# Kernel tuning notes

Hardware: AMD Instinct MI355X
Metric: run time of the kernel (lower is better)

The kernel has to match this reference:

```python
import jax, jax.numpy as jnp
import numpy as np
import math

B, D, N, H, NHEADS, NCLS = 4096, 256, 256, 1, 4, 10


def conv(x, w, b, stride, pad):
    y = jax.lax.conv_general_dilated(x, w, (stride, stride), [(pad, pad), (pad, pad)],
                                     dimension_numbers=('NCHW', 'OIHW', 'NCHW'))
    return y + b[None, :, None, None]


def cdist(z, c):
    # z: [B, D], c: [N, D] -> Euclidean distance [B, N]
    d2 = jnp.sum(z * z, -1)[:, None] + jnp.sum(c * c, -1)[None, :] - 2.0 * (z @ c.T)
    return jnp.sqrt(jnp.maximum(d2, 0.0))


def setup_inputs() -> dict:
    key = jax.random.key(0)
    ks = jax.random.split(key, 32)
    s = 0.02
    inp = {
        'x': jax.random.normal(ks[0], (B, 3, 32, 32), jnp.float32),
        'y': jax.random.randint(ks[1], (B,), 0, NCLS),
        'conv1_w': jax.random.normal(ks[2], (32, 3, 5, 5), jnp.float32) * s,
        'conv1_b': jnp.zeros((32,), jnp.float32),
        'conv2_w': jax.random.normal(ks[3], (64, 32, 3, 3), jnp.float32) * s,
        'conv2_b': jnp.zeros((64,), jnp.float32),
        'conv3_w': jax.random.normal(ks[4], (128, 64, 3, 3), jnp.float32) * s,
        'conv3_b': jnp.zeros((128,), jnp.float32),
        'conv4_w': jax.random.normal(ks[5], (256, 128, 3, 3), jnp.float32) * s,
        'conv4_b': jnp.zeros((256,), jnp.float32),
        'enc_w': jax.random.normal(ks[6], (256 * 8 * 8, D), jnp.float32) * s,
        'enc_b': jnp.zeros((D,), jnp.float32),
        'class_emb': jax.random.normal(ks[7], (NCLS, D), jnp.float32),
        'node_emb': jax.random.normal(ks[8], (N_NODES := 1, D), jnp.float32),
        'query_w': jax.random.normal(ks[9], (D, D), jnp.float32) * s,
        'query_b': jnp.zeros((D,), jnp.float32),
        'attn_w': jax.random.normal(ks[10], (D, D * NHEADS), jnp.float32) * s,
        'attn_b': jnp.zeros((D * NHEADS,), jnp.float32),
        'clf_w': jax.random.normal(ks[11], (D * NHEADS, NCLS), jnp.float32) * s,
        'clf_b': jnp.zeros((NCLS,), jnp.float32),
        'node_fc_w': jax.random.normal(ks[12], (D, D), jnp.float32) * s,
        'node_fc_b': jnp.zeros((D,), jnp.float32),
        'protos': jax.random.normal(ks[13], (N, D), jnp.float32),
        'grid_pos': jax.random.normal(ks[14], (N, D), jnp.float32),
        'temp_raw': jnp.array([math.log(0.95 / 0.05)], jnp.float32),
        'gate_logits': jnp.zeros((N,), jnp.float32),
    }
    return inp


def reference(x, y, conv1_w, conv1_b, conv2_w, conv2_b, conv3_w, conv3_b,
              conv4_w, conv4_b, enc_w, enc_b, class_emb, node_emb,
              query_w, query_b, attn_w, attn_b, clf_w, clf_b,
              node_fc_w, node_fc_b, protos, grid_pos, temp_raw, gate_logits):
    # shared encoder: conv stack -> flatten -> linear, 32x32 -> 8x8
    h1 = jax.nn.relu(conv(x, conv1_w, conv1_b, 2, 1))    # [B,32,15,15]
    h2 = jax.nn.relu(conv(h1, conv2_w, conv2_b, 2, 1))   # [B,64,8,8]
    h3 = jax.nn.relu(conv(h2, conv3_w, conv3_b, 1, 1))   # [B,128,8,8]
    h4 = jax.nn.relu(conv(h3, conv4_w, conv4_b, 1, 1))   # [B,256,8,8]
    z0 = h4.reshape(x.shape[0], -1) @ enc_w + enc_b      # [B,D]

    # Node: encoder_fc + SoftSOM (cdist + cdist -> softmax -> gate -> renorm -> blend)
    z = z0 @ node_fc_w + node_fc_b
    temp = jax.nn.sigmoid(temp_raw[0]) * (1.0 - 0.001) + 0.001
    d_total = cdist(z, protos) + cdist(z, grid_pos)      # [B,N]
    w = jax.nn.softmax(-d_total / temp, axis=-1) * jax.nn.sigmoid(gate_logits)[None, :]
    w = w / (w.sum(-1, keepdims=True) + 1e-8)
    blended = w @ protos                                 # [B,D]

    # node attention over n_nodes=1
    topo_stack = blended[:, None, :]                     # [B,1,D]
    query = class_emb[y] @ query_w + query_b             # [B,D]
    proj = (node_emb @ attn_w + attn_b).reshape(node_emb.shape[0], NHEADS, D)  # [n,h,D]
    attn_logits = jnp.einsum('bd,nhd->bhn', query, proj)
    attn_w_ = jax.nn.softmax(attn_logits, axis=-1)
    fused = jnp.einsum('bhn,bnd->bhd', attn_w_, topo_stack).reshape(x.shape[0], NHEADS * D)
    logits = fused @ clf_w + clf_b                       # [B,10]
    return logits
```

## Files before the change

kernel.cpp:

```cpp
#include <hip/hip_runtime.h>
#include <math.h>

#define TPB 256

typedef __attribute__((ext_vector_type(8))) short bf16x8;
typedef __attribute__((ext_vector_type(4))) float f32x4;
typedef __attribute__((ext_vector_type(2))) float f32x2;

#define OFF_PN2   0
#define OFF_GN2   256
#define OFF_GATE  512
#define OFF_TEMP  768
#define OFF_WEFF  1024
#define OFF_W1T   3584
#define OFF_W2T_BYTES 737280ul
#define OFF_W3T_BYTES 786432ul
#define OFF_W4T_BYTES 983040ul
#define OFF_EWT_BYTES 2097152ul
#define OFF_NFWT_BYTES 10485760ul
#define OFF_PJD_BYTES  10616832ul
#define OFF_GJD_BYTES  10747904ul
#define OFF_PTB_BYTES  10878976ul
#define OFF_A_BYTES   12582912ul
#define OFF_B_BYTES   (OFF_A_BYTES + 67108864ul)
#define OFF_Z0_BYTES  (OFF_B_BYTES + 33554432ul)

__device__ __forceinline__ float bf2f(ushort u) {
  return __uint_as_float(((unsigned)u) << 16);
}
__device__ __forceinline__ ushort f2bf(float f) {
  unsigned x = __float_as_uint(f);
  return (ushort)((x + 0x7fffu + ((x >> 16) & 1u)) >> 16);
}
__device__ __forceinline__ unsigned pack2(float a, float b) {
  return (unsigned)f2bf(a) | ((unsigned)f2bf(b) << 16);
}

__device__ __forceinline__ void gload_lds16(const ushort* g, ushort* l) {
  __builtin_amdgcn_global_load_lds(
      (const __attribute__((address_space(1))) unsigned int*)g,
      (__attribute__((address_space(3))) unsigned int*)l, 16, 0, 0);
}

__device__ __forceinline__ float block_sum(float v, float* red) {
  #pragma unroll
  for (int off = 32; off > 0; off >>= 1) v += __shfl_down(v, off, 64);
  int wid = threadIdx.x >> 6;
  __syncthreads();
  if ((threadIdx.x & 63) == 0) red[wid] = v;
  __syncthreads();
  return red[0] + red[1] + red[2] + red[3];
}

__global__ void __launch_bounds__(256) k_init(
    const float* __restrict__ ew,    ushort* __restrict__ ewt,
    const float* __restrict__ w1,    const float* __restrict__ w2,
    const float* __restrict__ w3,    const float* __restrict__ w4,
    float* __restrict__ w1t, ushort* __restrict__ w2t,
    ushort* __restrict__ w3t, ushort* __restrict__ w4t,
    const float* __restrict__ protos, const float* __restrict__ gridp,
    const float* __restrict__ gate_logits, const float* __restrict__ temp_raw,
    const float* __restrict__ clf_w, float* __restrict__ ws,
    const float* __restrict__ nfw, ushort* __restrict__ nfwt,
    ushort* __restrict__ pjd, ushort* __restrict__ gjd,
    ushort* __restrict__ ptb) {
  __shared__ float tile[64][65];
  __shared__ float red[4];
  const int bx = blockIdx.x, t = threadIdx.x;

  if (bx < 1024) {
    int kb = bx & 255, nb = bx >> 8;
    #pragma unroll
    for (int i = 0; i < 16; ++i) {
      int idx = t + i*256, k = idx >> 6, n = idx & 63;
      tile[k][n] = ew[(size_t)(kb*64 + k)*256 + nb*64 + n];
    }
    __syncthreads();
    #pragma unroll
    for (int i = 0; i < 16; ++i) {
      int idx = t + i*256, n = idx >> 6, k = idx & 63;
      ewt[(size_t)(nb*64 + n)*16384 + kb*64 + k] = f2bf(tile[k][n]);
    }
    return;
  }
  if (bx < 2176) {
    int idx = (bx - 1024)*256 + t;
    if (idx < 2400) {
      int tap = idx >> 5, oc = idx & 31;
      w1t[idx] = w1[oc*75 + tap];
    }
    if (idx < 18432) {
      int tap = idx >> 11, r = idx & 2047, oc = r >> 5, ic = r & 31;
      w2t[idx] = f2bf(w2[oc*288 + ic*9 + tap]);
    }
    if (idx < 73728) {
      int tap = idx >> 13, r = idx & 8191, oc = r >> 6, ic = r & 63;
      w3t[idx] = f2bf(w3[oc*576 + ic*9 + tap]);
    }
    if (idx < 294912) {
      int tap = idx >> 15, r = idx & 32767, oc = r >> 7, ic = r & 127;
      w4t[idx] = f2bf(w4[oc*1152 + ic*9 + tap]);
    }
    return;
  }
  if (bx < 2432) {
    int b = bx - 2176;
    float pv = protos[b*256 + t];
    float gv = gridp [b*256 + t];
    float sp = block_sum(pv*pv, red);
    float sg = block_sum(gv*gv, red);
    if (t == 0) {
      ws[OFF_PN2 + b] = sp;
      ws[OFF_GN2 + b] = sg;
      ws[OFF_GATE + b] = 1.f/(1.f + expf(-gate_logits[b]));
    }
    if (b == 0) {
      for (int i = t; i < 2560; i += TPB) {
        int d = i/10, c = i%10;
        ws[OFF_WEFF + i] = clf_w[d*10+c] + clf_w[(256+d)*10+c]
                         + clf_w[(512+d)*10+c] + clf_w[(768+d)*10+c];
      }
      if (t == 0) {
        float s = 1.f/(1.f + expf(-temp_raw[0]));
        ws[OFF_TEMP] = s*(1.f - 0.001f) + 0.001f;
      }
    }
    return;
  }
  {
    int idx = (bx - 2432)*256 + t;
    int a = idx >> 8, b = idx & 255;
    nfwt[idx] = f2bf(nfw[b*256 + a]);
    pjd [idx] = f2bf(protos[idx]);
    gjd [idx] = f2bf(gridp[idx]);
    ptb [idx] = f2bf(protos[b*256 + a]);
  }
}

__global__ void __launch_bounds__(256) k_conv12(const float* __restrict__ x,
    const float* __restrict__ w1t, const float* __restrict__ b1,
    const ushort* __restrict__ w2t, const float* __restrict__ b2,
    ushort* __restrict__ h2c) {
  __shared__ ushort xs[17*17*40];
  __shared__ float  xf[3*32*33];
  int b = blockIdx.x, t = threadIdx.x;
  for (int i = t; i < 5780; i += TPB) ((unsigned*)xs)[i] = 0u;
  const float* xb = x + (size_t)b*3072;
  #pragma unroll
  for (int i = 0; i < 3; ++i) {
    int idx = (t + i*256)*4;
    float4 v = *(const float4*)&xb[idx];
    int ic = idx >> 10, rem = idx & 1023, iy = rem >> 5, ix = rem & 31;
    float* dst = &xf[ic*1056 + iy*33 + ix];
    dst[0] = v.x; dst[1] = v.y; dst[2] = v.z; dst[3] = v.w;
  }
  __syncthreads();

  if (t < 225) {
    int oy = t/15, ox = t%15;
    f32x2 acc[16];
    #pragma unroll
    for (int o = 0; o < 16; ++o) acc[o] = *(const f32x2*)&b1[2*o];
    for (int ic = 0; ic < 3; ++ic) {
      const int icb = ic*1056;
      #pragma unroll
      for (int ky = 0; ky < 5; ++ky) {
        int iy = 2*oy - 1 + ky;
        bool rok = (unsigned)iy < 32u;
        int rbase = icb + (rok ? iy*33 : 0);
        #pragma unroll
        for (int kx = 0; kx < 5; ++kx) {
          int ix = 2*ox - 1 + kx;
          bool ok = rok && ((unsigned)ix < 32u);
          float xv = xf[rbase + (ok ? ix : 0)];
          xv = ok ? xv : 0.f;
          f32x2 xv2 = {xv, xv};
          const float* wrow = &w1t[(ic*25 + ky*5 + kx)*32];
          #pragma unroll
          for (int g = 0; g < 8; ++g) {
            f32x2 wlo = {wrow[4*g+0], wrow[4*g+1]};
            f32x2 whi = {wrow[4*g+2], wrow[4*g+3]};
            acc[2*g]   += xv2*wlo;
            acc[2*g+1] += xv2*whi;
          }
        }
      }
    }
    unsigned pk[16];
    #pragma unroll
    for (int g = 0; g < 16; ++g)
      pk[g] = pack2(fmaxf(acc[g].x, 0.f), fmaxf(acc[g].y, 0.f));
    ushort* cell = &xs[((oy+1)*17 + (ox+1))*40];
    #pragma unroll
    for (int q = 0; q < 4; ++q) *(uint4*)(cell + q*8) = ((uint4*)pk)[q];
  }
  __syncthreads();

  const int lane = t & 63, w = t >> 6;
  const int quad = lane >> 4, row16 = lane & 15;
  f32x4 acc2[4];
  #pragma unroll
  for (int mt = 0; mt < 4; ++mt) acc2[mt] = (f32x4)0.f;
  #pragma unroll
  for (int ky = 0; ky < 3; ++ky)
    #pragma unroll
    for (int kx = 0; kx < 3; ++kx) {
      int tap = ky*3 + kx;
      bf16x8 bf = *(const bf16x8*)&w2t[tap*2048 + (w*16 + row16)*32 + quad*8];
      #pragma unroll
      for (int mt = 0; mt < 4; ++mt) {
        int px = mt*16 + row16;
        int iy = 2*(px >> 3) + ky, ix = 2*(px & 7) + kx;
        bf16x8 af = *(const bf16x8*)&xs[(iy*17 + ix)*40 + quad*8];
        acc2[mt] = __builtin_amdgcn_mfma_f32_16x16x32_bf16(bf, af, acc2[mt], 0, 0, 0);
      }
    }
  float4 bb = *(const float4*)&b2[w*16 + quad*4];
  #pragma unroll
  for (int mt = 0; mt < 4; ++mt) {
    int px = mt*16 + row16;
    uint2 dd;
    dd.x = pack2(fmaxf(acc2[mt][0] + bb.x, 0.f), fmaxf(acc2[mt][1] + bb.y, 0.f));
    dd.y = pack2(fmaxf(acc2[mt][2] + bb.z, 0.f), fmaxf(acc2[mt][3] + bb.w, 0.f));
    *(uint2*)&h2c[(size_t)b*4096 + px*64 + w*16 + quad*4] = dd;
  }
}

__global__ void __launch_bounds__(256, 2) k_conv34(const ushort* __restrict__ h2c,
    const float* __restrict__ b3, const float* __restrict__ b4,
    const ushort* __restrict__ w3t, const ushort* __restrict__ w4t,
    ushort* __restrict__ h4c, int img_base) {
  __shared__ __attribute__((aligned(16))) ushort buf[27200];
  ushort* xp  = buf;
  ushort* h3p = buf;
  const int bl = blockIdx.x, t = threadIdx.x;

  for (int i = t; i < 648; i += 256) {
    int img = (i >= 324), r = i - img*324;
    int row = r/9, c = r - row*9;
    int rr = (row < 20) ? ((row < 10) ? row : row + 80)
                        : (((row-20) >> 1) + 1)*10 + ((row-20) & 1)*9;
    *(uint4*)&xp[img*7200 + rr*72 + c*8] = (uint4){0,0,0,0};
  }
  #pragma unroll
  for (int u = 0; u < 4; ++u) {
    int i = t + u*256;
    int img = i >> 9, px = (i >> 3) & 63, icg = i & 7;
    bf16x8 v = *(const bf16x8*)&h2c[(size_t)(img_base + bl*2 + img)*4096 + px*64 + icg*8];
    int row = ((px >> 3) + 1)*10 + (px & 7) + 1;
    *(bf16x8*)&xp[img*7200 + row*72 + icg*8] = v;
  }
  __syncthreads();

  const int lane = t & 63, w = t >> 6;
  const int quad = lane >> 4, row16 = lane & 15;

  int b3off[8], b4off[8], r11c[8];
  #pragma unroll
  for (int mt = 0; mt < 8; ++mt) {
    int px = (mt & 3)*16 + row16;
    int r00 = (px >> 3)*10 + (px & 7);
    int img = mt >> 2;
    b3off[mt] = img*7200  + r00*72  + quad*8;
    b4off[mt] = img*13600 + r00*136 + quad*8;
    r11c[mt]  = img*13600 + (r00 + 11)*136;
  }

  const int ocb3 = w*32;
  f32x4 c3[8][2];
  #pragma unroll
  for (int mt = 0; mt < 8; ++mt) { c3[mt][0] = (f32x4)0.f; c3[mt][1] = (f32x4)0.f; }
  const ushort* w3b = w3t + (ocb3 + row16)*64 + quad*8;
  bf16x8 wa0 = *(const bf16x8*)(w3b);
  bf16x8 wa1 = *(const bf16x8*)(w3b + 1024);
  #pragma unroll
  for (int tap = 0; tap < 9; ++tap) {
    const int t72 = ((tap/3)*10 + (tap%3))*72;
    #pragma unroll
    for (int ks = 0; ks < 2; ++ks) {
      const ushort* wn = w3b + ((ks == 0) ? (tap*8192 + 32) : ((tap+1)*8192));
      bf16x8 n0 = *(const bf16x8*)(wn);
      bf16x8 n1 = *(const bf16x8*)(wn + 1024);
      #pragma unroll
      for (int mt = 0; mt < 8; ++mt) {
        bf16x8 af = *(const bf16x8*)&xp[b3off[mt] + t72 + ks*32];
        c3[mt][0] = __builtin_amdgcn_mfma_f32_16x16x32_bf16(wa0, af, c3[mt][0], 0, 0, 0);
        c3[mt][1] = __builtin_amdgcn_mfma_f32_16x16x32_bf16(wa1, af, c3[mt][1], 0, 0, 0);
      }
      wa0 = n0; wa1 = n1;
    }
  }
  __syncthreads();

  for (int i = t; i < 1224; i += 256) {
    int img2 = (i >= 612), r = i - img2*612;
    int row = r/17, c = r - row*17;
    int rr = (row < 20) ? ((row < 10) ? row : row + 80)
                        : (((row-20) >> 1) + 1)*10 + ((row-20) & 1)*9;
    *(uint4*)&h3p[img2*13600 + rr*136 + c*8] = (uint4){0,0,0,0};
  }
  #pragma unroll
  for (int nt = 0; nt < 2; ++nt) {
    float4 bb = *(const float4*)&b3[ocb3 + nt*16 + quad*4];
    #pragma unroll
    for (int mt = 0; mt < 8; ++mt) {
      uint2 dd;
      dd.x = pack2(fmaxf(c3[mt][nt][0] + bb.x, 0.f), fmaxf(c3[mt][nt][1] + bb.y, 0.f));
      dd.y = pack2(fmaxf(c3[mt][nt][2] + bb.z, 0.f), fmaxf(c3[mt][nt][3] + bb.w, 0.f));
      *(uint2*)&h3p[r11c[mt] + ocb3 + nt*16 + quad*4] = dd;
    }
  }
  __syncthreads();

  const int ocb4 = w*64;
  f32x4 c4[8][4];
  #pragma unroll
  for (int mt = 0; mt < 8; ++mt)
    #pragma unroll
    for (int nt = 0; nt < 4; ++nt) c4[mt][nt] = (f32x4)0.f;
  const ushort* w4b = w4t + (ocb4 + row16)*128 + quad*8;
  bf16x8 r4[4];
  #pragma unroll
  for (int nt = 0; nt < 4; ++nt) r4[nt] = *(const bf16x8*)(w4b + nt*2048);
  #pragma unroll
  for (int tap = 0; tap < 9; ++tap) {
    const int t136 = ((tap/3)*10 + (tap%3))*136;
    #pragma unroll
    for (int ks = 0; ks < 4; ++ks) {
      const ushort* wn = w4b + ((ks < 3) ? (tap*32768 + (ks+1)*32) : ((tap+1)*32768));
      bf16x8 nx[4];
      #pragma unroll
      for (int nt = 0; nt < 4; ++nt) nx[nt] = *(const bf16x8*)(wn + nt*2048);
      #pragma unroll
      for (int mt = 0; mt < 8; ++mt) {
        bf16x8 ax = *(const bf16x8*)&h3p[b4off[mt] + t136 + ks*32];
        #pragma unroll
        for (int nt = 0; nt < 4; ++nt)
          c4[mt][nt] = __builtin_amdgcn_mfma_f32_16x16x32_bf16(ax, r4[nt], c4[mt][nt], 0, 0, 0);
      }
      #pragma unroll
      for (int nt = 0; nt < 4; ++nt) r4[nt] = nx[nt];
    }
  }
  #pragma unroll
  for (int nt = 0; nt < 4; ++nt) {
    int oc = ocb4 + nt*16 + row16;
    float bv = b4[oc];
    #pragma unroll
    for (int mt = 0; mt < 8; ++mt) {
      int ig = bl*2 + (mt >> 2);
      int px0 = (mt & 3)*16 + quad*4;
      uint2 dd;
      dd.x = pack2(fmaxf(c4[mt][nt][0] + bv, 0.f), fmaxf(c4[mt][nt][1] + bv, 0.f));
      dd.y = pack2(fmaxf(c4[mt][nt][2] + bv, 0.f), fmaxf(c4[mt][nt][3] + bv, 0.f));
      *(uint2*)&h4c[(size_t)ig*16384 + oc*64 + px0] = dd;
    }
  }
}

__global__ void __launch_bounds__(512) k_enc(const ushort* __restrict__ h4c,
    const ushort* __restrict__ ewt, float* __restrict__ z0p) {
  __shared__ ushort a_s[2][128*64];
  __shared__ ushort b_s[2][128*64];
  const int t = threadIdx.x, bid = blockIdx.x;
  const int slice = bid & 7;
  const int mb    = (bid >> 3) & 15;
  const int nb    = bid >> 7;
  const int M0 = mb*128, N0 = nb*128;
  const int kbase = slice*2048;
  const int lane = t & 63, wv = t >> 6;
  const int quad = lane >> 4, row16 = lane & 15;
  const int mrow0 = (wv & 3)*32, ncol0 = (wv >> 2)*64;
  const int sr = lane >> 3, sp = lane & 7;

  f32x4 acc[2][4];
  #pragma unroll
  for (int mt = 0; mt < 2; ++mt)
    #pragma unroll
    for (int nt = 0; nt < 4; ++nt) acc[mt][nt] = (f32x4)0.f;

  #pragma unroll
  for (int u = 0; u < 2; ++u) {
    int r = wv*16 + u*8 + sr;
    int c = sp ^ (r & 7);
    gload_lds16(&h4c[(size_t)(M0 + r)*16384 + kbase + c*8], &a_s[0][(wv*16 + u*8)*64]);
    gload_lds16(&ewt[(size_t)(N0 + r)*16384 + kbase + c*8], &b_s[0][(wv*16 + u*8)*64]);
  }
  __syncthreads();

  int cur = 0;
  for (int kt = 0; kt < 32; ++kt) {
    if (kt < 31) {
      const int k1 = kbase + (kt + 1)*64;
      #pragma unroll
      for (int u = 0; u < 2; ++u) {
        int r = wv*16 + u*8 + sr;
        int c = sp ^ (r & 7);
        gload_lds16(&h4c[(size_t)(M0 + r)*16384 + k1 + c*8], &a_s[cur^1][(wv*16 + u*8)*64]);
        gload_lds16(&ewt[(size_t)(N0 + r)*16384 + k1 + c*8], &b_s[cur^1][(wv*16 + u*8)*64]);
      }
    }
    #pragma unroll
    for (int ks = 0; ks < 2; ++ks) {
      bf16x8 af[2], bf[4];
      #pragma unroll
      for (int mt = 0; mt < 2; ++mt) {
        int r = mrow0 + mt*16 + row16;
        int p = (ks*4 + quad) ^ (r & 7);
        af[mt] = *(const bf16x8*)&a_s[cur][r*64 + p*8];
      }
      #pragma unroll
      for (int nt = 0; nt < 4; ++nt) {
        int r = ncol0 + nt*16 + row16;
        int p = (ks*4 + quad) ^ (r & 7);
        bf[nt] = *(const bf16x8*)&b_s[cur][r*64 + p*8];
      }
      #pragma unroll
      for (int mt = 0; mt < 2; ++mt)
        #pragma unroll
        for (int nt = 0; nt < 4; ++nt)
          acc[mt][nt] = __builtin_amdgcn_mfma_f32_16x16x32_bf16(af[mt], bf[nt], acc[mt][nt], 0, 0, 0);
    }
    __syncthreads();
    cur ^= 1;
  }
  #pragma unroll
  for (int mt = 0; mt < 2; ++mt) {
    int il = M0 + mrow0 + mt*16 + quad*4;
    #pragma unroll
    for (int nt = 0; nt < 4; ++nt) {
      int col = N0 + ncol0 + nt*16 + row16;
      #pragma unroll
      for (int r = 0; r < 4; ++r)
        z0p[((size_t)slice*2048 + il + r)*256 + col] = acc[mt][nt][r];
    }
  }
}

__global__ void __launch_bounds__(256) k_post2(const float* __restrict__ zp,
    const float* __restrict__ enc_b, const float* __restrict__ nfb,
    const ushort* __restrict__ nfwt, const ushort* __restrict__ pjd,
    const ushort* __restrict__ gjd, const ushort* __restrict__ ptb,
    const float* __restrict__ ws, const float* __restrict__ clf_b,
    float* __restrict__ out) {
  __shared__ ushort zin[16*264];
  __shared__ ushort zS [16*264];
  __shared__ float  Df [16*264];
  __shared__ ushort wS [16*264];
  __shared__ float  weffS[2560];
  __shared__ float  gateS[256], pnS[256], gnS[256];
  __shared__ float  z2s[16];
  const int t = threadIdx.x, bx = blockIdx.x;
  const int img0 = bx*16;
  gateS[t] = ws[OFF_GATE + t];
  pnS[t]   = ws[OFF_PN2 + t];
  gnS[t]   = ws[OFF_GN2 + t];
  #pragma unroll
  for (int u = 0; u < 10; ++u)
    weffS[t + u*256] = ws[OFF_WEFF + t + u*256];
  #pragma unroll
  for (int u = 0; u < 16; ++u) {
    int i = t + u*256;
    int im = i >> 8, d = i & 255;
    int img = img0 + im;
    int cc = img >> 11, il = img & 2047;
    const float* zb = zp + (size_t)cc*4194304 + (size_t)il*256 + d;
    float s = enc_b[d];
    #pragma unroll
    for (int s8 = 0; s8 < 8; ++s8) s += zb[(size_t)s8*524288];
    zin[im*264 + d] = f2bf(s);
  }
  __syncthreads();

  const int lane = t & 63, w = t >> 6;
  const int quad = lane >> 4, row16 = lane & 15;
  const int n0 = w*64;

  f32x4 zC[4];
  #pragma unroll
  for (int nt = 0; nt < 4; ++nt) zC[nt] = (f32x4)0.f;
  #pragma unroll
  for (int ks = 0; ks < 8; ++ks) {
    bf16x8 az = *(const bf16x8*)&zin[row16*264 + ks*32 + quad*8];
    #pragma unroll
    for (int nt = 0; nt < 4; ++nt) {
      bf16x8 bw = *(const bf16x8*)&nfwt[(n0 + nt*16 + row16)*256 + ks*32 + quad*8];
      zC[nt] = __builtin_amdgcn_mfma_f32_16x16x32_bf16(az, bw, zC[nt], 0, 0, 0);
    }
  }
  #pragma unroll
  for (int nt = 0; nt < 4; ++nt) {
    int n = n0 + nt*16 + row16;
    float nb = nfb[n];
    #pragma unroll
    for (int r = 0; r < 4; ++r)
      zS[(quad*4 + r)*264 + n] = f2bf(zC[nt][r] + nb);
  }
  __syncthreads();

  {
    int im = t >> 4, jg = t & 15;
    float s = 0.f;
    #pragma unroll
    for (int q = 0; q < 16; ++q) {
      float v = bf2f(zS[im*264 + jg + 16*q]);
      s += v*v;
    }
    #pragma unroll
    for (int off = 8; off; off >>= 1) s += __shfl_xor(s, off, 16);
    if (jg == 0) z2s[im] = s;
  }
  __syncthreads();

  f32x4 dpC[4], dgC[4];
  #pragma unroll
  for (int nt = 0; nt < 4; ++nt) { dpC[nt] = (f32x4)0.f; dgC[nt] = (f32x4)0.f; }
  #pragma unroll
  for (int ks = 0; ks < 8; ++ks) {
    bf16x8 az = *(const bf16x8*)&zS[row16*264 + ks*32 + quad*8];
    #pragma unroll
    for (int nt = 0; nt < 4; ++nt) {
      int j = n0 + nt*16 + row16;
      bf16x8 bp = *(const bf16x8*)&pjd[j*256 + ks*32 + quad*8];
      bf16x8 bg = *(const bf16x8*)&gjd[j*256 + ks*32 + quad*8];
      dpC[nt] = __builtin_amdgcn_mfma_f32_16x16x32_bf16(az, bp, dpC[nt], 0, 0, 0);
      dgC[nt] = __builtin_amdgcn_mfma_f32_16x16x32_bf16(az, bg, dgC[nt], 0, 0, 0);
    }
  }
  {
    float temp = ws[OFF_TEMP];
    #pragma unroll
    for (int nt = 0; nt < 4; ++nt) {
      int j = n0 + nt*16 + row16;
      float pn = pnS[j], gn = gnS[j];
      #pragma unroll
      for (int r = 0; r < 4; ++r) {
        int im = quad*4 + r;
        float z2 = z2s[im];
        float d2p = z2 + pn - 2.f*dpC[nt][r];
        float d2g = z2 + gn - 2.f*dgC[nt][r];
        float l = -(sqrtf(fmaxf(d2p, 0.f)) + sqrtf(fmaxf(d2g, 0.f)))/temp;
        Df[im*264 + j] = l;
      }
    }
  }
  __syncthreads();

  {
    int im = t >> 4, jg = t & 15;
    float m = -1e30f;
    #pragma unroll
    for (int q = 0; q < 16; ++q) m = fmaxf(m, Df[im*264 + jg + 16*q]);
    #pragma unroll
    for (int off = 8; off; off >>= 1) m = fmaxf(m, __shfl_xor(m, off, 16));
    float E = 0.f, S = 0.f, ev[16], gv[16];
    #pragma unroll
    for (int q = 0; q < 16; ++q) {
      int j = jg + 16*q;
      float e = expf(Df[im*264 + j] - m);
      float g = gateS[j];
      ev[q] = e; gv[q] = g;
      E += e; S += e*g;
    }
    #pragma unroll
    for (int off = 8; off; off >>= 1) {
      E += __shfl_xor(E, off, 16);
      S += __shfl_xor(S, off, 16);
    }
    float inv = 1.f/(S + 1e-8f*E);
    #pragma unroll
    for (int q = 0; q < 16; ++q)
      wS[im*264 + jg + 16*q] = f2bf(ev[q]*gv[q]*inv);
  }
  __syncthreads();

  f32x4 blC[4];
  #pragma unroll
  for (int nt = 0; nt < 4; ++nt) blC[nt] = (f32x4)0.f;
  #pragma unroll
  for (int ks = 0; ks < 8; ++ks) {
    bf16x8 aw = *(const bf16x8*)&wS[row16*264 + ks*32 + quad*8];
    #pragma unroll
    for (int nt = 0; nt < 4; ++nt) {
      bf16x8 bp = *(const bf16x8*)&ptb[(n0 + nt*16 + row16)*256 + ks*32 + quad*8];
      blC[nt] = __builtin_amdgcn_mfma_f32_16x16x32_bf16(aw, bp, blC[nt], 0, 0, 0);
    }
  }
  #pragma unroll
  for (int nt = 0; nt < 4; ++nt) {
    int d = n0 + nt*16 + row16;
    #pragma unroll
    for (int r = 0; r < 4; ++r)
      Df[(quad*4 + r)*264 + d] = blC[nt][r];
  }
  __syncthreads();

  if (t < 160) {
    int im = t/10, c = t - im*10;
    float s = clf_b[c];
    for (int d = 0; d < 256; ++d)
      s += Df[im*264 + d]*weffS[d*10 + c];
    out[(size_t)(img0 + im)*10 + c] = s;
  }
}

extern "C" void kernel_launch(void* const* d_in, const int* in_sizes, int n_in,
                              void* d_out, int out_size, void* d_ws, size_t ws_size,
                              hipStream_t stream) {
  (void)in_sizes; (void)n_in; (void)out_size; (void)ws_size;
  const float* x      = (const float*)d_in[0];
  const float* c1w    = (const float*)d_in[2];
  const float* c1b    = (const float*)d_in[3];
  const float* c2w    = (const float*)d_in[4];
  const float* c2b    = (const float*)d_in[5];
  const float* c3w    = (const float*)d_in[6];
  const float* c3b    = (const float*)d_in[7];
  const float* c4w    = (const float*)d_in[8];
  const float* c4b    = (const float*)d_in[9];
  const float* encw   = (const float*)d_in[10];
  const float* encb   = (const float*)d_in[11];
  const float* clfw   = (const float*)d_in[18];
  const float* clfb   = (const float*)d_in[19];
  const float* nfw    = (const float*)d_in[20];
  const float* nfb    = (const float*)d_in[21];
  const float* protos = (const float*)d_in[22];
  const float* gridp  = (const float*)d_in[23];
  const float* traw   = (const float*)d_in[24];
  const float* gatel  = (const float*)d_in[25];

  float*  ws   = (float*)d_ws;
  float*  w1t  = ws + OFF_W1T;
  ushort* w2t  = (ushort*)((char*)d_ws + OFF_W2T_BYTES);
  ushort* w3t  = (ushort*)((char*)d_ws + OFF_W3T_BYTES);
  ushort* w4t  = (ushort*)((char*)d_ws + OFF_W4T_BYTES);
  ushort* ewt  = (ushort*)((char*)d_ws + OFF_EWT_BYTES);
  ushort* nfwt = (ushort*)((char*)d_ws + OFF_NFWT_BYTES);
  ushort* pjd  = (ushort*)((char*)d_ws + OFF_PJD_BYTES);
  ushort* gjd  = (ushort*)((char*)d_ws + OFF_GJD_BYTES);
  ushort* ptb  = (ushort*)((char*)d_ws + OFF_PTB_BYTES);
  ushort* h4c  = (ushort*)((char*)d_ws + OFF_A_BYTES);
  ushort* h2c  = (ushort*)((char*)d_ws + OFF_B_BYTES);
  float*  zp   = (float*) ((char*)d_ws + OFF_B_BYTES);
  float*  out  = (float*)d_out;

  hipLaunchKernelGGL(k_init, dim3(2688), dim3(TPB), 0, stream,
                     encw, ewt, c1w, c2w, c3w, c4w, w1t, w2t, w3t, w4t,
                     protos, gridp, gatel, traw, clfw, ws,
                     nfw, nfwt, pjd, gjd, ptb);
  hipLaunchKernelGGL(k_conv12, dim3(4096), dim3(TPB), 0, stream, x, w1t, c1b, w2t, c2b, h2c);
  for (int c = 0; c < 2; ++c) {
    hipLaunchKernelGGL(k_conv34, dim3(1024), dim3(TPB), 0, stream,
                       h2c, c3b, c4b, w3t, w4t, h4c, c*2048);
    hipLaunchKernelGGL(k_enc, dim3(256), dim3(512), 0, stream,
                       h4c, ewt, zp + (size_t)c*4194304);
  }
  hipLaunchKernelGGL(k_post2, dim3(256), dim3(TPB), 0, stream,
                     zp, encb, nfb, nfwt, pjd, gjd, ptb, ws, clfb, out);
}
```

Measured before the change: 495.2 us.

## Co-schedule second half of conv1-2 with first conv3-4 chunk in one launch

The conv1/conv2 stage is split into two halves of 2048 images. The second half runs inside the same grid as the first conv3/conv4 chunk, with block index selecting which body runs, so the two independent stages can occupy the GPU together instead of running back to back. Conv bodies are moved into inline device functions so both kernels can share them. The trade-off is that conv1/conv2 blocks in the fused kernel reserve the larger conv3/conv4 shared-memory footprint and inherit its launch bounds, which may lower their occupancy.

```diff
diff --git a/kernel.cpp b/kernel.cpp
--- a/kernel.cpp
+++ b/kernel.cpp
@@ -52,98 +52,12 @@
   return red[0] + red[1] + red[2] + red[3];
 }
 
-__global__ void __launch_bounds__(256) k_init(
-    const float* __restrict__ ew,    ushort* __restrict__ ewt,
-    const float* __restrict__ w1,    const float* __restrict__ w2,
-    const float* __restrict__ w3,    const float* __restrict__ w4,
-    float* __restrict__ w1t, ushort* __restrict__ w2t,
-    ushort* __restrict__ w3t, ushort* __restrict__ w4t,
-    const float* __restrict__ protos, const float* __restrict__ gridp,
-    const float* __restrict__ gate_logits, const float* __restrict__ temp_raw,
-    const float* __restrict__ clf_w, float* __restrict__ ws,
-    const float* __restrict__ nfw, ushort* __restrict__ nfwt,
-    ushort* __restrict__ pjd, ushort* __restrict__ gjd,
-    ushort* __restrict__ ptb) {
-  __shared__ float tile[64][65];
-  __shared__ float red[4];
-  const int bx = blockIdx.x, t = threadIdx.x;
-
-  if (bx < 1024) {
-    int kb = bx & 255, nb = bx >> 8;
-    #pragma unroll
-    for (int i = 0; i < 16; ++i) {
-      int idx = t + i*256, k = idx >> 6, n = idx & 63;
-      tile[k][n] = ew[(size_t)(kb*64 + k)*256 + nb*64 + n];
-    }
-    __syncthreads();
-    #pragma unroll
-    for (int i = 0; i < 16; ++i) {
-      int idx = t + i*256, n = idx >> 6, k = idx & 63;
-      ewt[(size_t)(nb*64 + n)*16384 + kb*64 + k] = f2bf(tile[k][n]);
-    }
-    return;
-  }
-  if (bx < 2176) {
-    int idx = (bx - 1024)*256 + t;
-    if (idx < 2400) {
-      int tap = idx >> 5, oc = idx & 31;
-      w1t[idx] = w1[oc*75 + tap];
-    }
-    if (idx < 18432) {
-      int tap = idx >> 11, r = idx & 2047, oc = r >> 5, ic = r & 31;
-      w2t[idx] = f2bf(w2[oc*288 + ic*9 + tap]);
-    }
-    if (idx < 73728) {
-      int tap = idx >> 13, r = idx & 8191, oc = r >> 6, ic = r & 63;
-      w3t[idx] = f2bf(w3[oc*576 + ic*9 + tap]);
-    }
-    if (idx < 294912) {
-      int tap = idx >> 15, r = idx & 32767, oc = r >> 7, ic = r & 127;
-      w4t[idx] = f2bf(w4[oc*1152 + ic*9 + tap]);
-    }
-    return;
-  }
-  if (bx < 2432) {
-    int b = bx - 2176;
-    float pv = protos[b*256 + t];
-    float gv = gridp [b*256 + t];
-    float sp = block_sum(pv*pv, red);
-    float sg = block_sum(gv*gv, red);
-    if (t == 0) {
-      ws[OFF_PN2 + b] = sp;
-      ws[OFF_GN2 + b] = sg;
-      ws[OFF_GATE + b] = 1.f/(1.f + expf(-gate_logits[b]));
-    }
-    if (b == 0) {
-      for (int i = t; i < 2560; i += TPB) {
-        int d = i/10, c = i%10;
-        ws[OFF_WEFF + i] = clf_w[d*10+c] + clf_w[(256+d)*10+c]
-                         + clf_w[(512+d)*10+c] + clf_w[(768+d)*10+c];
-      }
-      if (t == 0) {
-        float s = 1.f/(1.f + expf(-temp_raw[0]));
-        ws[OFF_TEMP] = s*(1.f - 0.001f) + 0.001f;
-      }
-    }
-    return;
-  }
-  {
-    int idx = (bx - 2432)*256 + t;
-    int a = idx >> 8, b = idx & 255;
-    nfwt[idx] = f2bf(nfw[b*256 + a]);
-    pjd [idx] = f2bf(protos[idx]);
-    gjd [idx] = f2bf(gridp[idx]);
-    ptb [idx] = f2bf(protos[b*256 + a]);
-  }
-}
-
-__global__ void __launch_bounds__(256) k_conv12(const float* __restrict__ x,
-    const float* __restrict__ w1t, const float* __restrict__ b1,
-    const ushort* __restrict__ w2t, const float* __restrict__ b2,
-    ushort* __restrict__ h2c) {
-  __shared__ ushort xs[17*17*40];
-  __shared__ float  xf[3*32*33];
-  int b = blockIdx.x, t = threadIdx.x;
+
+__device__ __forceinline__ void conv12_body(int b, int t,
+    const float* __restrict__ x, const float* __restrict__ w1t,
+    const float* __restrict__ b1, const ushort* __restrict__ w2t,
+    const float* __restrict__ b2, ushort* __restrict__ h2c,
+    ushort* xs, float* xf) {
   for (int i = t; i < 5780; i += TPB) ((unsigned*)xs)[i] = 0u;
   const float* xb = x + (size_t)b*3072;
   #pragma unroll
@@ -226,14 +140,13 @@
   }
 }
 
-__global__ void __launch_bounds__(256, 2) k_conv34(const ushort* __restrict__ h2c,
-    const float* __restrict__ b3, const float* __restrict__ b4,
-    const ushort* __restrict__ w3t, const ushort* __restrict__ w4t,
-    ushort* __restrict__ h4c, int img_base) {
-  __shared__ __attribute__((aligned(16))) ushort buf[27200];
+__device__ __forceinline__ void conv34_body(int bl, int t,
+    const ushort* __restrict__ h2c, const float* __restrict__ b3,
+    const float* __restrict__ b4, const ushort* __restrict__ w3t,
+    const ushort* __restrict__ w4t, ushort* __restrict__ h4c,
+    int img_base, ushort* buf) {
   ushort* xp  = buf;
   ushort* h3p = buf;
-  const int bl = blockIdx.x, t = threadIdx.x;
 
   for (int i = t; i < 648; i += 256) {
     int img = (i >= 324), r = i - img*324;
@@ -356,6 +269,126 @@
       *(uint2*)&h4c[(size_t)ig*16384 + oc*64 + px0] = dd;
     }
   }
+}
+
+__global__ void __launch_bounds__(256) k_init(
+    const float* __restrict__ ew,    ushort* __restrict__ ewt,
+    const float* __restrict__ w1,    const float* __restrict__ w2,
+    const float* __restrict__ w3,    const float* __restrict__ w4,
+    float* __restrict__ w1t, ushort* __restrict__ w2t,
+    ushort* __restrict__ w3t, ushort* __restrict__ w4t,
+    const float* __restrict__ protos, const float* __restrict__ gridp,
+    const float* __restrict__ gate_logits, const float* __restrict__ temp_raw,
+    const float* __restrict__ clf_w, float* __restrict__ ws,
+    const float* __restrict__ nfw, ushort* __restrict__ nfwt,
+    ushort* __restrict__ pjd, ushort* __restrict__ gjd,
+    ushort* __restrict__ ptb) {
+  __shared__ float tile[64][65];
+  __shared__ float red[4];
+  const int bx = blockIdx.x, t = threadIdx.x;
+
+  if (bx < 1024) {
+    int kb = bx & 255, nb = bx >> 8;
+    #pragma unroll
+    for (int i = 0; i < 16; ++i) {
+      int idx = t + i*256, k = idx >> 6, n = idx & 63;
+      tile[k][n] = ew[(size_t)(kb*64 + k)*256 + nb*64 + n];
+    }
+    __syncthreads();
+    #pragma unroll
+    for (int i = 0; i < 16; ++i) {
+      int idx = t + i*256, n = idx >> 6, k = idx & 63;
+      ewt[(size_t)(nb*64 + n)*16384 + kb*64 + k] = f2bf(tile[k][n]);
+    }
+    return;
+  }
+  if (bx < 2176) {
+    int idx = (bx - 1024)*256 + t;
+    if (idx < 2400) {
+      int tap = idx >> 5, oc = idx & 31;
+      w1t[idx] = w1[oc*75 + tap];
+    }
+    if (idx < 18432) {
+      int tap = idx >> 11, r = idx & 2047, oc = r >> 5, ic = r & 31;
+      w2t[idx] = f2bf(w2[oc*288 + ic*9 + tap]);
+    }
+    if (idx < 73728) {
+      int tap = idx >> 13, r = idx & 8191, oc = r >> 6, ic = r & 63;
+      w3t[idx] = f2bf(w3[oc*576 + ic*9 + tap]);
+    }
+    if (idx < 294912) {
+      int tap = idx >> 15, r = idx & 32767, oc = r >> 7, ic = r & 127;
+      w4t[idx] = f2bf(w4[oc*1152 + ic*9 + tap]);
+    }
+    return;
+  }
+  if (bx < 2432) {
+    int b = bx - 2176;
+    float pv = protos[b*256 + t];
+    float gv = gridp [b*256 + t];
+    float sp = block_sum(pv*pv, red);
+    float sg = block_sum(gv*gv, red);
+    if (t == 0) {
+      ws[OFF_PN2 + b] = sp;
+      ws[OFF_GN2 + b] = sg;
+      ws[OFF_GATE + b] = 1.f/(1.f + expf(-gate_logits[b]));
+    }
+    if (b == 0) {
+      for (int i = t; i < 2560; i += TPB) {
+        int d = i/10, c = i%10;
+        ws[OFF_WEFF + i] = clf_w[d*10+c] + clf_w[(256+d)*10+c]
+                         + clf_w[(512+d)*10+c] + clf_w[(768+d)*10+c];
+      }
+      if (t == 0) {
+        float s = 1.f/(1.f + expf(-temp_raw[0]));
+        ws[OFF_TEMP] = s*(1.f - 0.001f) + 0.001f;
+      }
+    }
+    return;
+  }
+  {
+    int idx = (bx - 2432)*256 + t;
+    int a = idx >> 8, b = idx & 255;
+    nfwt[idx] = f2bf(nfw[b*256 + a]);
+    pjd [idx] = f2bf(protos[idx]);
+    gjd [idx] = f2bf(gridp[idx]);
+    ptb [idx] = f2bf(protos[b*256 + a]);
+  }
+}
+
+__global__ void __launch_bounds__(256) k_conv12(const float* __restrict__ x,
+    const float* __restrict__ w1t, const float* __restrict__ b1,
+    const ushort* __restrict__ w2t, const float* __restrict__ b2,
+    ushort* __restrict__ h2c, int img_base) {
+  __shared__ __attribute__((aligned(16))) ushort xs[11560];
+  __shared__ float xf[3168];
+  conv12_body(img_base + blockIdx.x, threadIdx.x, x, w1t, b1, w2t, b2, h2c, xs, xf);
+}
+
+__global__ void __launch_bounds__(256, 2) k_c34c12(const ushort* __restrict__ h2c,
+    const float* __restrict__ b3, const float* __restrict__ b4,
+    const ushort* __restrict__ w3t, const ushort* __restrict__ w4t,
+    ushort* __restrict__ h4c,
+    const float* __restrict__ x, const float* __restrict__ w1t,
+    const float* __restrict__ b1, const ushort* __restrict__ w2t,
+    const float* __restrict__ b2, ushort* __restrict__ h2c_out) {
+  __shared__ __attribute__((aligned(16))) ushort buf[27200];
+  const int bx = blockIdx.x, t = threadIdx.x;
+  if (bx < 1024) {
+    conv34_body(bx, t, h2c, b3, b4, w3t, w4t, h4c, 0, buf);
+  } else {
+    ushort* xs = buf;
+    float*  xf = (float*)(buf + 11560);
+    conv12_body(2048 + (bx - 1024), t, x, w1t, b1, w2t, b2, h2c_out, xs, xf);
+  }
+}
+
+__global__ void __launch_bounds__(256, 2) k_conv34(const ushort* __restrict__ h2c,
+    const float* __restrict__ b3, const float* __restrict__ b4,
+    const ushort* __restrict__ w3t, const ushort* __restrict__ w4t,
+    ushort* __restrict__ h4c, int img_base) {
+  __shared__ __attribute__((aligned(16))) ushort buf[27200];
+  conv34_body(blockIdx.x, threadIdx.x, h2c, b3, b4, w3t, w4t, h4c, img_base, buf);
 }
 
 __global__ void __launch_bounds__(512) k_enc(const ushort* __restrict__ h4c,
@@ -647,13 +680,17 @@
                      encw, ewt, c1w, c2w, c3w, c4w, w1t, w2t, w3t, w4t,
                      protos, gridp, gatel, traw, clfw, ws,
                      nfw, nfwt, pjd, gjd, ptb);
-  hipLaunchKernelGGL(k_conv12, dim3(4096), dim3(TPB), 0, stream, x, w1t, c1b, w2t, c2b, h2c);
-  for (int c = 0; c < 2; ++c) {
-    hipLaunchKernelGGL(k_conv34, dim3(1024), dim3(TPB), 0, stream,
-                       h2c, c3b, c4b, w3t, w4t, h4c, c*2048);
-    hipLaunchKernelGGL(k_enc, dim3(256), dim3(512), 0, stream,
-                       h4c, ewt, zp + (size_t)c*4194304);
-  }
+  hipLaunchKernelGGL(k_conv12, dim3(2048), dim3(TPB), 0, stream,
+                     x, w1t, c1b, w2t, c2b, h2c, 0);
+  hipLaunchKernelGGL(k_c34c12, dim3(3072), dim3(TPB), 0, stream,
+                     h2c, c3b, c4b, w3t, w4t, h4c,
+                     x, w1t, c1b, w2t, c2b, h2c);
+  hipLaunchKernelGGL(k_enc, dim3(256), dim3(512), 0, stream,
+                     h4c, ewt, zp);
+  hipLaunchKernelGGL(k_conv34, dim3(1024), dim3(TPB), 0, stream,
+                     h2c, c3b, c4b, w3t, w4t, h4c, 2048);
+  hipLaunchKernelGGL(k_enc, dim3(256), dim3(512), 0, stream,
+                     h4c, ewt, zp + (size_t)1*4194304);
   hipLaunchKernelGGL(k_post2, dim3(256), dim3(TPB), 0, stream,
                      zp, encb, nfb, nfwt, pjd, gjd, ptb, ws, clfb, out);
 }
```

Measured after the change: 857.4 us. 73.1% more time.
